# Optimization experiments

Hardware: AMD Instinct MI355X
Metric: run time of the kernel (lower is better)

## Reference

```python
import jax, jax.numpy as jnp
import numpy as np

NUM_Q = 4        # len(n_e_list)
N_E = 2048       # codes per quantizer level
E_DIM = 128      # e_dim
N_TOK = 32768    # flattened tokens
BETA = 0.25      # commitment coefficient


def setup_inputs() -> dict:
    key = jax.random.key(0)
    k_x, k_cb = jax.random.split(key)
    x = jax.random.normal(k_x, (N_TOK, E_DIM), dtype=jnp.float32)
    codebooks = jax.random.normal(k_cb, (NUM_Q, N_E, E_DIM), dtype=jnp.float32) * 0.1
    return {"x": x, "codebooks": codebooks, "use_freq": 0}


def _vq_layer(res, cb):
    # res: [N, D], cb: [K, D]
    # squared euclidean distance via expansion: ||r||^2 - 2 r.c + ||c||^2
    d = (jnp.sum(res * res, axis=-1, keepdims=True)
         - 2.0 * (res @ cb.T)
         + jnp.sum(cb * cb, axis=-1))            # [N, K]
    idx = jnp.argmin(d, axis=-1)                  # [N]
    q = cb[idx]                                   # [N, D] gather
    sg = jax.lax.stop_gradient
    # VQ-VAE loss: codebook term + beta * commitment term
    loss = jnp.mean((q - sg(res)) ** 2) + BETA * jnp.mean((sg(q) - res) ** 2)
    q_st = res + sg(q - res)                      # straight-through estimator
    return q_st, loss, idx


def reference(x, codebooks, use_freq):
    # residual chain over NUM_Q quantizer levels (sequential dependency)
    def step(carry, cb):
        residual, x_q = carry
        q, loss, idx = _vq_layer(residual, cb)
        return (residual - q, x_q + q), (loss, idx)

    (residual, x_q), (losses, indices) = jax.lax.scan(
        step, (x, jnp.zeros_like(x)), codebooks)
    mean_loss = jnp.mean(losses)
    all_indices = jnp.moveaxis(indices, 0, -1)    # [N, NUM_Q]
    return x_q, mean_loss, all_indices
```

## Files before the change

### kernel.cpp

```cpp
#include <hip/hip_runtime.h>

#define NTOK 32768
#define NE   2048
#define EDIM 128
#define NQ   4

#define TOKT 64
#define CHCODES 64
#define NCHUNK (NE / CHCODES)
#define CAP 16
#define MARGIN 0.25f

typedef __attribute__((ext_vector_type(8))) short short8v;
typedef __attribute__((ext_vector_type(4))) float f32x4;

__device__ __forceinline__ unsigned short bf16rne(float x) {
    unsigned u = __float_as_uint(x);
    unsigned r = 0x7FFFu + ((u >> 16) & 1u);
    return (unsigned short)((u + r) >> 16);
}

__device__ __forceinline__ void gld16(const void* g, const void* l) {
    __builtin_amdgcn_global_load_lds(
        (const __attribute__((address_space(1))) unsigned int*)g,
        (__attribute__((address_space(3))) unsigned int*)l, 16, 0, 0);
}

#define MFMA_BF16 __builtin_amdgcn_mfma_f32_16x16x32_bf16

__global__ __launch_bounds__(256) void prep_kernel(
    const float* __restrict__ cb, unsigned short* __restrict__ cb16s,
    float* __restrict__ cnorm, float* __restrict__ loss_accum)
{
    const int row = blockIdx.x * 256 + threadIdx.x;
    if (row == 0) *loss_accum = 0.0f;
    const float* src = cb + (size_t)row * EDIM;
    unsigned short* dst = cb16s + (size_t)row * EDIM;
    const int swz8 = (row & 7) << 3;
    float s = 0.0f;
#pragma unroll
    for (int j = 0; j < EDIM / 4; ++j) {
        float4 v = ((const float4*)src)[j];
        s += v.x * v.x; s += v.y * v.y; s += v.z * v.z; s += v.w * v.w;
        ushort4 o;
        o.x = bf16rne(v.x); o.y = bf16rne(v.y);
        o.z = bf16rne(v.z); o.w = bf16rne(v.w);
        *(ushort4*)(dst + ((j * 4) ^ swz8)) = o;
    }
    cnorm[row] = s;
}

__global__ __launch_bounds__(256, 2) void vq_level_kernel(
    const float* __restrict__ rin,
    const float* __restrict__ cbF,
    const unsigned short* __restrict__ cbL,
    const float* __restrict__ cnorm,
    float* __restrict__ rout,
    float* __restrict__ xq,
    float* __restrict__ idx_out,
    float* __restrict__ loss_accum,
    int level, int first)
{
    __shared__ __align__(16) float Af[TOKT][132];
    __shared__ __align__(16) unsigned short Bs[2][CHCODES * EDIM];
    __shared__ float part[4 * TOKT];
    __shared__ float rns[TOKT];
    __shared__ float mdw[2][TOKT];
    __shared__ int   cnt[TOKT];
    __shared__ int   lst[TOKT * CAP];
    __shared__ float redb_d[4][TOKT];
    __shared__ int   redb_i[4][TOKT];
    __shared__ int   idx_s[TOKT];
    __shared__ float lsum[256];

    const int t     = threadIdx.x;
    const int tok0  = blockIdx.x * TOKT;
    const int w     = t >> 6;
    const int rh    = w >> 1;
    const int chalf = w & 1;
    const int cl    = t & 15;
    const int lg    = (t & 63) >> 4;
    if (t < TOKT) cnt[t] = 0;

    {
        const int tok = t & 63;
        const int dg  = t >> 6;
        float s = 0.0f;
#pragma unroll
        for (int j = 0; j < 8; ++j) {
            const int d0 = dg * 32 + j * 4;
            float4 v = *(const float4*)(rin + (size_t)(tok0 + tok) * EDIM + d0);
            *(float4*)&Af[tok][d0] = v;
            s += v.x * v.x; s += v.y * v.y; s += v.z * v.z; s += v.w * v.w;
        }
        part[dg * TOKT + tok] = s;
    }
    __syncthreads();
    if (t < TOKT)
        rns[t] = ((part[t] + part[TOKT + t]) + part[2 * TOKT + t])
                 + part[3 * TOKT + t];

    short8v a00, a01, a02, a03, a10, a11, a12, a13;
#define LDA(AF, AROW, KT) { \
    float4 p0 = *(const float4*)&Af[AROW][(KT) * 32 + lg * 8]; \
    float4 p1 = *(const float4*)&Af[AROW][(KT) * 32 + lg * 8 + 4]; \
    AF[0] = (short)bf16rne(p0.x); AF[1] = (short)bf16rne(p0.y); \
    AF[2] = (short)bf16rne(p0.z); AF[3] = (short)bf16rne(p0.w); \
    AF[4] = (short)bf16rne(p1.x); AF[5] = (short)bf16rne(p1.y); \
    AF[6] = (short)bf16rne(p1.z); AF[7] = (short)bf16rne(p1.w); }
    {
        const int ar0 = rh * 32 + cl, ar1 = rh * 32 + 16 + cl;
        LDA(a00, ar0, 0) LDA(a01, ar0, 1) LDA(a02, ar0, 2) LDA(a03, ar0, 3)
        LDA(a10, ar1, 0) LDA(a11, ar1, 1) LDA(a12, ar1, 2) LDA(a13, ar1, 3)
    }
#undef LDA

    const int swzk = (cl & 7) << 4;
    const int inn0 = (0   + lg * 16) ^ swzk;
    const int inn1 = (64  + lg * 16) ^ swzk;
    const int inn2 = (128 + lg * 16) ^ swzk;
    const int inn3 = (192 + lg * 16) ^ swzk;

#define STAGE(DST, CH) { \
    const char* gs = (const char*)cbL + (size_t)(CH) * 16384 + t * 16; \
    char* ls = (char*)(DST) + (t & 192) * 16; \
    gld16(gs,         ls); \
    gld16(gs + 4096,  ls + 4096); \
    gld16(gs + 8192,  ls + 8192); \
    gld16(gs + 12288, ls + 12288); }

#define MFMAG(BUFC, CH, CT, TAIL) { \
    const char* bp = (const char*)&Bs[BUFC][0] \
                     + (chalf * 32 + (CT) * 16 + cl) * 256; \
    short8v b0 = *(const short8v*)(bp + inn0); \
    short8v b1 = *(const short8v*)(bp + inn1); \
    short8v b2 = *(const short8v*)(bp + inn2); \
    short8v b3 = *(const short8v*)(bp + inn3); \
    f32x4 ac0 = {0.f, 0.f, 0.f, 0.f}; \
    f32x4 ac1 = {0.f, 0.f, 0.f, 0.f}; \
    ac0 = MFMA_BF16(a00, b0, ac0, 0, 0, 0); \
    ac0 = MFMA_BF16(a01, b1, ac0, 0, 0, 0); \
    ac0 = MFMA_BF16(a02, b2, ac0, 0, 0, 0); \
    ac0 = MFMA_BF16(a03, b3, ac0, 0, 0, 0); \
    ac1 = MFMA_BF16(a10, b0, ac1, 0, 0, 0); \
    ac1 = MFMA_BF16(a11, b1, ac1, 0, 0, 0); \
    ac1 = MFMA_BF16(a12, b2, ac1, 0, 0, 0); \
    ac1 = MFMA_BF16(a13, b3, ac1, 0, 0, 0); \
    const int code = (CH) * CHCODES + chalf * 32 + (CT) * 16 + cl; \
    const float cn = cnorm[code]; \
    TAIL }

#define T_MIN \
    md00 = fminf(md00, (rn00 - 2.f * ac0[0]) + cn); \
    md01 = fminf(md01, (rn01 - 2.f * ac0[1]) + cn); \
    md02 = fminf(md02, (rn02 - 2.f * ac0[2]) + cn); \
    md03 = fminf(md03, (rn03 - 2.f * ac0[3]) + cn); \
    md10 = fminf(md10, (rn10 - 2.f * ac1[0]) + cn); \
    md11 = fminf(md11, (rn11 - 2.f * ac1[1]) + cn); \
    md12 = fminf(md12, (rn12 - 2.f * ac1[2]) + cn); \
    md13 = fminf(md13, (rn13 - 2.f * ac1[3]) + cn);

#define PUSH(AC, R, RN, TH, TOKB) { \
    float dd = ((RN) - 2.f * AC[R]) + cn; \
    if (dd < (TH)) { int p = atomicAdd(&cnt[(TOKB) + R], 1); \
                     if (p < CAP) lst[((TOKB) + R) * CAP + p] = code; } }
#define T_CAND \
    PUSH(ac0, 0, rn00, th00, tokb0) PUSH(ac0, 1, rn01, th01, tokb0) \
    PUSH(ac0, 2, rn02, th02, tokb0) PUSH(ac0, 3, rn03, th03, tokb0) \
    PUSH(ac1, 0, rn10, th10, tokb1) PUSH(ac1, 1, rn11, th11, tokb1) \
    PUSH(ac1, 2, rn12, th12, tokb1) PUSH(ac1, 3, rn13, th13, tokb1)

#define CH_P1(B, CH) { MFMAG(B, CH, 0, T_MIN)  MFMAG(B, CH, 1, T_MIN)  }
#define CH_P2(B, CH) { MFMAG(B, CH, 0, T_CAND) MFMAG(B, CH, 1, T_CAND) }

    STAGE(&Bs[0][0], 0)
    __syncthreads();

    const int tokb0 = rh * 32 + lg * 4;
    const int tokb1 = tokb0 + 16;
    const float rn00 = rns[tokb0 + 0], rn01 = rns[tokb0 + 1];
    const float rn02 = rns[tokb0 + 2], rn03 = rns[tokb0 + 3];
    const float rn10 = rns[tokb1 + 0], rn11 = rns[tokb1 + 1];
    const float rn12 = rns[tokb1 + 2], rn13 = rns[tokb1 + 3];

    float md00 = 3.402823466e38f, md01 = md00, md02 = md00, md03 = md00;
    float md10 = md00, md11 = md00, md12 = md00, md13 = md00;

    for (int c2 = 0; c2 < NCHUNK / 2; ++c2) {
        const int c = c2 * 2;
        STAGE(&Bs[1][0], c + 1)
        CH_P1(0, c)
        __syncthreads();
        if (c + 2 < NCHUNK) STAGE(&Bs[0][0], c + 2)
        CH_P1(1, c + 1)
        __syncthreads();
    }

#pragma unroll
    for (int m = 1; m < 16; m <<= 1) {
        md00 = fminf(md00, __shfl_xor(md00, m, 64));
        md01 = fminf(md01, __shfl_xor(md01, m, 64));
        md02 = fminf(md02, __shfl_xor(md02, m, 64));
        md03 = fminf(md03, __shfl_xor(md03, m, 64));
        md10 = fminf(md10, __shfl_xor(md10, m, 64));
        md11 = fminf(md11, __shfl_xor(md11, m, 64));
        md12 = fminf(md12, __shfl_xor(md12, m, 64));
        md13 = fminf(md13, __shfl_xor(md13, m, 64));
    }
    if (cl == 0) {
        mdw[chalf][tokb0 + 0] = md00; mdw[chalf][tokb0 + 1] = md01;
        mdw[chalf][tokb0 + 2] = md02; mdw[chalf][tokb0 + 3] = md03;
        mdw[chalf][tokb1 + 0] = md10; mdw[chalf][tokb1 + 1] = md11;
        mdw[chalf][tokb1 + 2] = md12; mdw[chalf][tokb1 + 3] = md13;
    }

    STAGE(&Bs[0][0], 0)
    __syncthreads();

    const float th00 = fminf(mdw[0][tokb0 + 0], mdw[1][tokb0 + 0]) + MARGIN;
    const float th01 = fminf(mdw[0][tokb0 + 1], mdw[1][tokb0 + 1]) + MARGIN;
    const float th02 = fminf(mdw[0][tokb0 + 2], mdw[1][tokb0 + 2]) + MARGIN;
    const float th03 = fminf(mdw[0][tokb0 + 3], mdw[1][tokb0 + 3]) + MARGIN;
    const float th10 = fminf(mdw[0][tokb1 + 0], mdw[1][tokb1 + 0]) + MARGIN;
    const float th11 = fminf(mdw[0][tokb1 + 1], mdw[1][tokb1 + 1]) + MARGIN;
    const float th12 = fminf(mdw[0][tokb1 + 2], mdw[1][tokb1 + 2]) + MARGIN;
    const float th13 = fminf(mdw[0][tokb1 + 3], mdw[1][tokb1 + 3]) + MARGIN;

    for (int c2 = 0; c2 < NCHUNK / 2; ++c2) {
        const int c = c2 * 2;
        STAGE(&Bs[1][0], c + 1)
        CH_P2(0, c)
        __syncthreads();
        if (c + 2 < NCHUNK) STAGE(&Bs[0][0], c + 2)
        CH_P2(1, c + 1)
        __syncthreads();
    }

    {
        const int tok = t & 63;
        const int s   = t >> 6;
        const int n   = min(cnt[tok], CAP);
        const float rn_t = rns[tok];
        float bd = 3.402823466e38f;
        int   bi = 0x7fffffff;
        for (int i = s; i < n; i += 4) {
            const int c = lst[tok * CAP + i];
            const float* cr = cbF + (size_t)c * EDIM;
            float dot = 0.0f;
#pragma unroll 8
            for (int d = 0; d < EDIM; ++d)
                dot = fmaf(Af[tok][d], cr[d], dot);
            const float dd = (rn_t - 2.0f * dot) + cnorm[c];
            if (dd < bd || (dd == bd && c < bi)) { bd = dd; bi = c; }
        }
        redb_d[s][tok] = bd;
        redb_i[s][tok] = bi;
    }
    __syncthreads();
    if (t < TOKT) {
        float bd = redb_d[0][t];
        int   bi = redb_i[0][t];
#pragma unroll
        for (int s = 1; s < 4; ++s) {
            const float dd = redb_d[s][t];
            const int   ii = redb_i[s][t];
            if (dd < bd || (dd == bd && ii < bi)) { bd = dd; bi = ii; }
        }
        idx_s[t] = bi;
        idx_out[(size_t)(tok0 + t) * NQ + level] = (float)bi;
    }
    __syncthreads();

    {
        const int tok = t >> 2;
        const int dq  = t & 3;
        const int gi  = idx_s[tok];
        const float* qrow = cbF + (size_t)gi * EDIM;
        float lp = 0.0f;
#pragma unroll
        for (int k = 0; k < 8; ++k) {
            const int d0 = k * 16 + dq * 4;
            const float4 q = *(const float4*)(qrow + d0);
            const float4 r = *(const float4*)&Af[tok][d0];
            float4 tq, qst, rnv;
            tq.x = q.x - r.x; tq.y = q.y - r.y; tq.z = q.z - r.z; tq.w = q.w - r.w;
            qst.x = r.x + tq.x; qst.y = r.y + tq.y;
            qst.z = r.z + tq.z; qst.w = r.w + tq.w;
            rnv.x = r.x - qst.x; rnv.y = r.y - qst.y;
            rnv.z = r.z - qst.z; rnv.w = r.w - qst.w;
            const size_t go = (size_t)(tok0 + tok) * EDIM + d0;
            *(float4*)(rout + go) = rnv;
            if (first) {
                *(float4*)(xq + go) = qst;
            } else {
                float4 o = *(const float4*)(xq + go);
                o.x += qst.x; o.y += qst.y; o.z += qst.z; o.w += qst.w;
                *(float4*)(xq + go) = o;
            }
            lp += tq.x * tq.x; lp += tq.y * tq.y;
            lp += tq.z * tq.z; lp += tq.w * tq.w;
        }
        lsum[t] = lp;
    }
    __syncthreads();
#pragma unroll
    for (int s2 = 128; s2 > 0; s2 >>= 1) {
        if (t < s2) lsum[t] += lsum[t + s2];
        __syncthreads();
    }
    if (t == 0) atomicAdd(loss_accum, lsum[0]);
}

__global__ void finalize_kernel(const float* __restrict__ loss_accum,
                                float* __restrict__ out_loss)
{
    *out_loss = *loss_accum * (1.25f / (4.0f * (float)NTOK * (float)EDIM));
}

extern "C" void kernel_launch(void* const* d_in, const int* in_sizes, int n_in,
                              void* d_out, int out_size, void* d_ws, size_t ws_size,
                              hipStream_t stream)
{
    const float* x  = (const float*)d_in[0];
    const float* cb = (const float*)d_in[1];

    float* out      = (float*)d_out;
    float* xq       = out;
    float* out_loss = out + (size_t)NTOK * EDIM;
    float* idx_out  = out + (size_t)NTOK * EDIM + 1;

    float* ws             = (float*)d_ws;
    float* cnorm          = ws;
    float* loss_accum     = ws + 8192;
    unsigned short* cb16s = (unsigned short*)(ws + 8448);
    float* r0             = ws + 8448 + (size_t)NQ * NE * EDIM / 2;

    prep_kernel<<<(NQ * NE) / 256, 256, 0, stream>>>(cb, cb16s, cnorm, loss_accum);

    for (int l = 0; l < NQ; ++l) {
        const float* rin = (l == 0) ? x : r0;
        vq_level_kernel<<<NTOK / TOKT, 256, 0, stream>>>(
            rin, cb + (size_t)l * NE * EDIM,
            cb16s + (size_t)l * NE * EDIM,
            cnorm + (size_t)l * NE,
            r0, xq, idx_out, loss_accum, l, (l == 0) ? 1 : 0);
    }
    finalize_kernel<<<1, 1, 0, stream>>>(loss_accum, out_loss);
}
```

Measured before the change: 291.7 us.

## Fuse all quantizer levels into one kernel keeping residual in LDS

Replaces the four per-level kernel launches with a single kernel that loops over the quantizer levels. The residual for each token tile now stays in shared memory between levels, and its norm is recomputed there, so the residual no longer round-trips through global memory. This removes per-level launch gaps and the residual read/write traffic. In exchange the long-running blocks lose the inter-level launch boundaries, and register pressure from the loop may rise.

```diff
diff --git a/kernel.cpp b/kernel.cpp
--- a/kernel.cpp
+++ b/kernel.cpp
@@ -50,16 +50,14 @@
     cnorm[row] = s;
 }
 
-__global__ __launch_bounds__(256, 2) void vq_level_kernel(
-    const float* __restrict__ rin,
-    const float* __restrict__ cbF,
-    const unsigned short* __restrict__ cbL,
-    const float* __restrict__ cnorm,
-    float* __restrict__ rout,
+__global__ __launch_bounds__(256, 2) void vq_fused_kernel(
+    const float* __restrict__ x,
+    const float* __restrict__ cbF0,
+    const unsigned short* __restrict__ cbL0,
+    const float* __restrict__ cnorm0,
     float* __restrict__ xq,
     float* __restrict__ idx_out,
-    float* __restrict__ loss_accum,
-    int level, int first)
+    float* __restrict__ loss_accum)
 {
     __shared__ __align__(16) float Af[TOKT][132];
     __shared__ __align__(16) unsigned short Bs[2][CHCODES * EDIM];
@@ -80,7 +78,6 @@
     const int chalf = w & 1;
     const int cl    = t & 15;
     const int lg    = (t & 63) >> 4;
-    if (t < TOKT) cnt[t] = 0;
 
     {
         const int tok = t & 63;
@@ -89,37 +86,22 @@
 #pragma unroll
         for (int j = 0; j < 8; ++j) {
             const int d0 = dg * 32 + j * 4;
-            float4 v = *(const float4*)(rin + (size_t)(tok0 + tok) * EDIM + d0);
+            float4 v = *(const float4*)(x + (size_t)(tok0 + tok) * EDIM + d0);
             *(float4*)&Af[tok][d0] = v;
             s += v.x * v.x; s += v.y * v.y; s += v.z * v.z; s += v.w * v.w;
         }
         part[dg * TOKT + tok] = s;
     }
     __syncthreads();
-    if (t < TOKT)
-        rns[t] = ((part[t] + part[TOKT + t]) + part[2 * TOKT + t])
-                 + part[3 * TOKT + t];
-
-    short8v a00, a01, a02, a03, a10, a11, a12, a13;
-#define LDA(AF, AROW, KT) { \
-    float4 p0 = *(const float4*)&Af[AROW][(KT) * 32 + lg * 8]; \
-    float4 p1 = *(const float4*)&Af[AROW][(KT) * 32 + lg * 8 + 4]; \
-    AF[0] = (short)bf16rne(p0.x); AF[1] = (short)bf16rne(p0.y); \
-    AF[2] = (short)bf16rne(p0.z); AF[3] = (short)bf16rne(p0.w); \
-    AF[4] = (short)bf16rne(p1.x); AF[5] = (short)bf16rne(p1.y); \
-    AF[6] = (short)bf16rne(p1.z); AF[7] = (short)bf16rne(p1.w); }
-    {
-        const int ar0 = rh * 32 + cl, ar1 = rh * 32 + 16 + cl;
-        LDA(a00, ar0, 0) LDA(a01, ar0, 1) LDA(a02, ar0, 2) LDA(a03, ar0, 3)
-        LDA(a10, ar1, 0) LDA(a11, ar1, 1) LDA(a12, ar1, 2) LDA(a13, ar1, 3)
-    }
-#undef LDA
 
     const int swzk = (cl & 7) << 4;
     const int inn0 = (0   + lg * 16) ^ swzk;
     const int inn1 = (64  + lg * 16) ^ swzk;
     const int inn2 = (128 + lg * 16) ^ swzk;
     const int inn3 = (192 + lg * 16) ^ swzk;
+
+    const int tokb0 = rh * 32 + lg * 4;
+    const int tokb1 = tokb0 + 16;
 
 #define STAGE(DST, CH) { \
     const char* gs = (const char*)cbL + (size_t)(CH) * 16384 + t * 16; \
@@ -173,142 +155,184 @@
 #define CH_P1(B, CH) { MFMAG(B, CH, 0, T_MIN)  MFMAG(B, CH, 1, T_MIN)  }
 #define CH_P2(B, CH) { MFMAG(B, CH, 0, T_CAND) MFMAG(B, CH, 1, T_CAND) }
 
-    STAGE(&Bs[0][0], 0)
-    __syncthreads();
-
-    const int tokb0 = rh * 32 + lg * 4;
-    const int tokb1 = tokb0 + 16;
-    const float rn00 = rns[tokb0 + 0], rn01 = rns[tokb0 + 1];
-    const float rn02 = rns[tokb0 + 2], rn03 = rns[tokb0 + 3];
-    const float rn10 = rns[tokb1 + 0], rn11 = rns[tokb1 + 1];
-    const float rn12 = rns[tokb1 + 2], rn13 = rns[tokb1 + 3];
-
-    float md00 = 3.402823466e38f, md01 = md00, md02 = md00, md03 = md00;
-    float md10 = md00, md11 = md00, md12 = md00, md13 = md00;
-
-    for (int c2 = 0; c2 < NCHUNK / 2; ++c2) {
-        const int c = c2 * 2;
-        STAGE(&Bs[1][0], c + 1)
-        CH_P1(0, c)
-        __syncthreads();
-        if (c + 2 < NCHUNK) STAGE(&Bs[0][0], c + 2)
-        CH_P1(1, c + 1)
+#pragma unroll 1
+    for (int l = 0; l < NQ; ++l) {
+        const float* cbF          = cbF0 + (size_t)l * NE * EDIM;
+        const unsigned short* cbL = cbL0 + (size_t)l * NE * EDIM;
+        const float* cnorm        = cnorm0 + (size_t)l * NE;
+
+        if (t < TOKT) {
+            rns[t] = ((part[t] + part[TOKT + t]) + part[2 * TOKT + t])
+                     + part[3 * TOKT + t];
+            cnt[t] = 0;
+        }
+
+        short8v a00, a01, a02, a03, a10, a11, a12, a13;
+#define LDA(AF, AROW, KT) { \
+    float4 p0 = *(const float4*)&Af[AROW][(KT) * 32 + lg * 8]; \
+    float4 p1 = *(const float4*)&Af[AROW][(KT) * 32 + lg * 8 + 4]; \
+    AF[0] = (short)bf16rne(p0.x); AF[1] = (short)bf16rne(p0.y); \
+    AF[2] = (short)bf16rne(p0.z); AF[3] = (short)bf16rne(p0.w); \
+    AF[4] = (short)bf16rne(p1.x); AF[5] = (short)bf16rne(p1.y); \
+    AF[6] = (short)bf16rne(p1.z); AF[7] = (short)bf16rne(p1.w); }
+        {
+            const int ar0 = rh * 32 + cl, ar1 = rh * 32 + 16 + cl;
+            LDA(a00, ar0, 0) LDA(a01, ar0, 1) LDA(a02, ar0, 2) LDA(a03, ar0, 3)
+            LDA(a10, ar1, 0) LDA(a11, ar1, 1) LDA(a12, ar1, 2) LDA(a13, ar1, 3)
+        }
+#undef LDA
+
+        STAGE(&Bs[0][0], 0)
+        __syncthreads();
+
+        const float rn00 = rns[tokb0 + 0], rn01 = rns[tokb0 + 1];
+        const float rn02 = rns[tokb0 + 2], rn03 = rns[tokb0 + 3];
+        const float rn10 = rns[tokb1 + 0], rn11 = rns[tokb1 + 1];
+        const float rn12 = rns[tokb1 + 2], rn13 = rns[tokb1 + 3];
+
+        float md00 = 3.402823466e38f, md01 = md00, md02 = md00, md03 = md00;
+        float md10 = md00, md11 = md00, md12 = md00, md13 = md00;
+
+        for (int c2 = 0; c2 < NCHUNK / 2; ++c2) {
+            const int c = c2 * 2;
+            STAGE(&Bs[1][0], c + 1)
+            CH_P1(0, c)
+            __syncthreads();
+            if (c + 2 < NCHUNK) STAGE(&Bs[0][0], c + 2)
+            CH_P1(1, c + 1)
+            __syncthreads();
+        }
+
+#pragma unroll
+        for (int m = 1; m < 16; m <<= 1) {
+            md00 = fminf(md00, __shfl_xor(md00, m, 64));
+            md01 = fminf(md01, __shfl_xor(md01, m, 64));
+            md02 = fminf(md02, __shfl_xor(md02, m, 64));
+            md03 = fminf(md03, __shfl_xor(md03, m, 64));
+            md10 = fminf(md10, __shfl_xor(md10, m, 64));
+            md11 = fminf(md11, __shfl_xor(md11, m, 64));
+            md12 = fminf(md12, __shfl_xor(md12, m, 64));
+            md13 = fminf(md13, __shfl_xor(md13, m, 64));
+        }
+        if (cl == 0) {
+            mdw[chalf][tokb0 + 0] = md00; mdw[chalf][tokb0 + 1] = md01;
+            mdw[chalf][tokb0 + 2] = md02; mdw[chalf][tokb0 + 3] = md03;
+            mdw[chalf][tokb1 + 0] = md10; mdw[chalf][tokb1 + 1] = md11;
+            mdw[chalf][tokb1 + 2] = md12; mdw[chalf][tokb1 + 3] = md13;
+        }
+
+        STAGE(&Bs[0][0], 0)
+        __syncthreads();
+
+        const float th00 = fminf(mdw[0][tokb0 + 0], mdw[1][tokb0 + 0]) + MARGIN;
+        const float th01 = fminf(mdw[0][tokb0 + 1], mdw[1][tokb0 + 1]) + MARGIN;
+        const float th02 = fminf(mdw[0][tokb0 + 2], mdw[1][tokb0 + 2]) + MARGIN;
+        const float th03 = fminf(mdw[0][tokb0 + 3], mdw[1][tokb0 + 3]) + MARGIN;
+        const float th10 = fminf(mdw[0][tokb1 + 0], mdw[1][tokb1 + 0]) + MARGIN;
+        const float th11 = fminf(mdw[0][tokb1 + 1], mdw[1][tokb1 + 1]) + MARGIN;
+        const float th12 = fminf(mdw[0][tokb1 + 2], mdw[1][tokb1 + 2]) + MARGIN;
+        const float th13 = fminf(mdw[0][tokb1 + 3], mdw[1][tokb1 + 3]) + MARGIN;
+
+        for (int c2 = 0; c2 < NCHUNK / 2; ++c2) {
+            const int c = c2 * 2;
+            STAGE(&Bs[1][0], c + 1)
+            CH_P2(0, c)
+            __syncthreads();
+            if (c + 2 < NCHUNK) STAGE(&Bs[0][0], c + 2)
+            CH_P2(1, c + 1)
+            __syncthreads();
+        }
+
+        {
+            const int tok = t & 63;
+            const int s   = t >> 6;
+            const int n   = min(cnt[tok], CAP);
+            const float rn_t = rns[tok];
+            float bd = 3.402823466e38f;
+            int   bi = 0x7fffffff;
+            for (int i = s; i < n; i += 4) {
+                const int c = lst[tok * CAP + i];
+                const float* cr = cbF + (size_t)c * EDIM;
+                float dot = 0.0f;
+#pragma unroll 8
+                for (int d = 0; d < EDIM; ++d)
+                    dot = fmaf(Af[tok][d], cr[d], dot);
+                const float dd = (rn_t - 2.0f * dot) + cnorm[c];
+                if (dd < bd || (dd == bd && c < bi)) { bd = dd; bi = c; }
+            }
+            redb_d[s][tok] = bd;
+            redb_i[s][tok] = bi;
+        }
+        __syncthreads();
+        if (t < TOKT) {
+            float bd = redb_d[0][t];
+            int   bi = redb_i[0][t];
+#pragma unroll
+            for (int s = 1; s < 4; ++s) {
+                const float dd = redb_d[s][t];
+                const int   ii = redb_i[s][t];
+                if (dd < bd || (dd == bd && ii < bi)) { bd = dd; bi = ii; }
+            }
+            idx_s[t] = bi;
+            idx_out[(size_t)(tok0 + t) * NQ + l] = (float)bi;
+        }
+        __syncthreads();
+
+        {
+            const int tok = t >> 2;
+            const int dq  = t & 3;
+            const int gi  = idx_s[tok];
+            const float* qrow = cbF + (size_t)gi * EDIM;
+            float lp = 0.0f;
+#pragma unroll
+            for (int k = 0; k < 8; ++k) {
+                const int d0 = k * 16 + dq * 4;
+                const float4 q = *(const float4*)(qrow + d0);
+                const float4 r = *(const float4*)&Af[tok][d0];
+                float4 tq, qst, rnv;
+                tq.x = q.x - r.x; tq.y = q.y - r.y;
+                tq.z = q.z - r.z; tq.w = q.w - r.w;
+                qst.x = r.x + tq.x; qst.y = r.y + tq.y;
+                qst.z = r.z + tq.z; qst.w = r.w + tq.w;
+                rnv.x = r.x - qst.x; rnv.y = r.y - qst.y;
+                rnv.z = r.z - qst.z; rnv.w = r.w - qst.w;
+                *(float4*)&Af[tok][d0] = rnv;
+                const size_t go = (size_t)(tok0 + tok) * EDIM + d0;
+                if (l == 0) {
+                    *(float4*)(xq + go) = qst;
+                } else {
+                    float4 o = *(const float4*)(xq + go);
+                    o.x += qst.x; o.y += qst.y; o.z += qst.z; o.w += qst.w;
+                    *(float4*)(xq + go) = o;
+                }
+                lp += tq.x * tq.x; lp += tq.y * tq.y;
+                lp += tq.z * tq.z; lp += tq.w * tq.w;
+            }
+            lsum[t] = lp;
+        }
+        __syncthreads();
+#pragma unroll
+        for (int s2 = 128; s2 > 0; s2 >>= 1) {
+            if (t < s2) lsum[t] += lsum[t + s2];
+            __syncthreads();
+        }
+        if (t == 0) atomicAdd(loss_accum, lsum[0]);
+
+        if (l + 1 < NQ) {
+            const int tok = t & 63;
+            const int dg  = t >> 6;
+            float s = 0.0f;
+#pragma unroll
+            for (int j = 0; j < 8; ++j) {
+                const int d0 = dg * 32 + j * 4;
+                const float4 v = *(const float4*)&Af[tok][d0];
+                s += v.x * v.x; s += v.y * v.y;
+                s += v.z * v.z; s += v.w * v.w;
+            }
+            part[dg * TOKT + tok] = s;
+        }
         __syncthreads();
     }
-
-#pragma unroll
-    for (int m = 1; m < 16; m <<= 1) {
-        md00 = fminf(md00, __shfl_xor(md00, m, 64));
-        md01 = fminf(md01, __shfl_xor(md01, m, 64));
-        md02 = fminf(md02, __shfl_xor(md02, m, 64));
-        md03 = fminf(md03, __shfl_xor(md03, m, 64));
-        md10 = fminf(md10, __shfl_xor(md10, m, 64));
-        md11 = fminf(md11, __shfl_xor(md11, m, 64));
-        md12 = fminf(md12, __shfl_xor(md12, m, 64));
-        md13 = fminf(md13, __shfl_xor(md13, m, 64));
-    }
-    if (cl == 0) {
-        mdw[chalf][tokb0 + 0] = md00; mdw[chalf][tokb0 + 1] = md01;
-        mdw[chalf][tokb0 + 2] = md02; mdw[chalf][tokb0 + 3] = md03;
-        mdw[chalf][tokb1 + 0] = md10; mdw[chalf][tokb1 + 1] = md11;
-        mdw[chalf][tokb1 + 2] = md12; mdw[chalf][tokb1 + 3] = md13;
-    }
-
-    STAGE(&Bs[0][0], 0)
-    __syncthreads();
-
-    const float th00 = fminf(mdw[0][tokb0 + 0], mdw[1][tokb0 + 0]) + MARGIN;
-    const float th01 = fminf(mdw[0][tokb0 + 1], mdw[1][tokb0 + 1]) + MARGIN;
-    const float th02 = fminf(mdw[0][tokb0 + 2], mdw[1][tokb0 + 2]) + MARGIN;
-    const float th03 = fminf(mdw[0][tokb0 + 3], mdw[1][tokb0 + 3]) + MARGIN;
-    const float th10 = fminf(mdw[0][tokb1 + 0], mdw[1][tokb1 + 0]) + MARGIN;
-    const float th11 = fminf(mdw[0][tokb1 + 1], mdw[1][tokb1 + 1]) + MARGIN;
-    const float th12 = fminf(mdw[0][tokb1 + 2], mdw[1][tokb1 + 2]) + MARGIN;
-    const float th13 = fminf(mdw[0][tokb1 + 3], mdw[1][tokb1 + 3]) + MARGIN;
-
-    for (int c2 = 0; c2 < NCHUNK / 2; ++c2) {
-        const int c = c2 * 2;
-        STAGE(&Bs[1][0], c + 1)
-        CH_P2(0, c)
-        __syncthreads();
-        if (c + 2 < NCHUNK) STAGE(&Bs[0][0], c + 2)
-        CH_P2(1, c + 1)
-        __syncthreads();
-    }
-
-    {
-        const int tok = t & 63;
-        const int s   = t >> 6;
-        const int n   = min(cnt[tok], CAP);
-        const float rn_t = rns[tok];
-        float bd = 3.402823466e38f;
-        int   bi = 0x7fffffff;
-        for (int i = s; i < n; i += 4) {
-            const int c = lst[tok * CAP + i];
-            const float* cr = cbF + (size_t)c * EDIM;
-            float dot = 0.0f;
-#pragma unroll 8
-            for (int d = 0; d < EDIM; ++d)
-                dot = fmaf(Af[tok][d], cr[d], dot);
-            const float dd = (rn_t - 2.0f * dot) + cnorm[c];
-            if (dd < bd || (dd == bd && c < bi)) { bd = dd; bi = c; }
-        }
-        redb_d[s][tok] = bd;
-        redb_i[s][tok] = bi;
-    }
-    __syncthreads();
-    if (t < TOKT) {
-        float bd = redb_d[0][t];
-        int   bi = redb_i[0][t];
-#pragma unroll
-        for (int s = 1; s < 4; ++s) {
-            const float dd = redb_d[s][t];
-            const int   ii = redb_i[s][t];
-            if (dd < bd || (dd == bd && ii < bi)) { bd = dd; bi = ii; }
-        }
-        idx_s[t] = bi;
-        idx_out[(size_t)(tok0 + t) * NQ + level] = (float)bi;
-    }
-    __syncthreads();
-
-    {
-        const int tok = t >> 2;
-        const int dq  = t & 3;
-        const int gi  = idx_s[tok];
-        const float* qrow = cbF + (size_t)gi * EDIM;
-        float lp = 0.0f;
-#pragma unroll
-        for (int k = 0; k < 8; ++k) {
-            const int d0 = k * 16 + dq * 4;
-            const float4 q = *(const float4*)(qrow + d0);
-            const float4 r = *(const float4*)&Af[tok][d0];
-            float4 tq, qst, rnv;
-            tq.x = q.x - r.x; tq.y = q.y - r.y; tq.z = q.z - r.z; tq.w = q.w - r.w;
-            qst.x = r.x + tq.x; qst.y = r.y + tq.y;
-            qst.z = r.z + tq.z; qst.w = r.w + tq.w;
-            rnv.x = r.x - qst.x; rnv.y = r.y - qst.y;
-            rnv.z = r.z - qst.z; rnv.w = r.w - qst.w;
-            const size_t go = (size_t)(tok0 + tok) * EDIM + d0;
-            *(float4*)(rout + go) = rnv;
-            if (first) {
-                *(float4*)(xq + go) = qst;
-            } else {
-                float4 o = *(const float4*)(xq + go);
-                o.x += qst.x; o.y += qst.y; o.z += qst.z; o.w += qst.w;
-                *(float4*)(xq + go) = o;
-            }
-            lp += tq.x * tq.x; lp += tq.y * tq.y;
-            lp += tq.z * tq.z; lp += tq.w * tq.w;
-        }
-        lsum[t] = lp;
-    }
-    __syncthreads();
-#pragma unroll
-    for (int s2 = 128; s2 > 0; s2 >>= 1) {
-        if (t < s2) lsum[t] += lsum[t + s2];
-        __syncthreads();
-    }
-    if (t == 0) atomicAdd(loss_accum, lsum[0]);
 }
 
 __global__ void finalize_kernel(const float* __restrict__ loss_accum,
@@ -333,17 +357,11 @@
     float* cnorm          = ws;
     float* loss_accum     = ws + 8192;
     unsigned short* cb16s = (unsigned short*)(ws + 8448);
-    float* r0             = ws + 8448 + (size_t)NQ * NE * EDIM / 2;
 
     prep_kernel<<<(NQ * NE) / 256, 256, 0, stream>>>(cb, cb16s, cnorm, loss_accum);
 
-    for (int l = 0; l < NQ; ++l) {
-        const float* rin = (l == 0) ? x : r0;
-        vq_level_kernel<<<NTOK / TOKT, 256, 0, stream>>>(
-            rin, cb + (size_t)l * NE * EDIM,
-            cb16s + (size_t)l * NE * EDIM,
-            cnorm + (size_t)l * NE,
-            r0, xq, idx_out, loss_accum, l, (l == 0) ? 1 : 0);
-    }
+    vq_fused_kernel<<<NTOK / TOKT, 256, 0, stream>>>(
+        x, cb, cb16s, cnorm, xq, idx_out, loss_accum);
+
     finalize_kernel<<<1, 1, 0, stream>>>(loss_accum, out_loss);
 }
```

Measured after the change: 261.7 us. -10.3%, faster.
